# Kernel optimization log

Measured on AMD Instinct MI355X. Metric: run time of the kernel, lower is better.

## Reference

```python
import jax, jax.numpy as jnp
import numpy as np

N_NODES = 50000
N_EDGES = 800000
D = 128


def setup_inputs() -> dict:
    key = jax.random.key(0)
    ks = jax.random.split(key, 6)
    node_features = jax.random.normal(ks[0], (N_NODES, D), dtype=jnp.float32)
    edge_index = jax.random.randint(ks[1], (2, N_EDGES), 0, N_NODES, dtype=jnp.int64)
    s = 1.0 / np.sqrt(D)
    W1 = jax.random.normal(ks[2], (D, D), dtype=jnp.float32) * s
    b1 = jnp.zeros((D,), dtype=jnp.float32)
    W2 = jax.random.normal(ks[3], (D, D), dtype=jnp.float32) * s
    b2 = jnp.zeros((D,), dtype=jnp.float32)
    eta = jax.random.normal(ks[4], (1, 1), dtype=jnp.float32) * 0.5
    ln_gamma = jnp.ones((D,), dtype=jnp.float32)
    ln_beta = jnp.zeros((D,), dtype=jnp.float32)
    return {"node_features": node_features, "edge_index": edge_index,
            "W1": W1, "b1": b1, "W2": W2, "b2": b2, "eta": eta,
            "ln_gamma": ln_gamma, "ln_beta": ln_beta}


def _layer_norm(x, gamma, beta, eps=1e-5):
    mu = jnp.mean(x, axis=-1, keepdims=True)
    var = jnp.var(x, axis=-1, keepdims=True)
    return (x - mu) * jax.lax.rsqrt(var + eps) * gamma + beta


def reference(node_features, edge_index, W1, b1, W2, b2, eta, ln_gamma, ln_beta):
    initial = node_features
    src, dst = edge_index[0], edge_index[1]
    # gather neighbor features and sum-aggregate per destination node
    hu = node_features[src]                                   # [E, D]
    sum_hu = jax.ops.segment_sum(hu, dst, num_segments=node_features.shape[0])
    z = (1.0 + eta) * node_features + sum_hu                  # [N, D]
    # MLP: Linear -> ReLU -> Linear -> ReLU, then outer ReLU (idempotent)
    h = jax.nn.relu(z @ W1.T + b1)
    h = jax.nn.relu(h @ W2.T + b2)
    h = jax.nn.relu(h)
    h = _layer_norm(h, ln_gamma, ln_beta)                     # dropout p=0 -> identity
    return h + initial                                        # skip connection
```

## Files before the change

### kernel.cpp

```cpp
#include <hip/hip_runtime.h>

#define NN 50000
#define NE 800000
#define DD 128

typedef unsigned int u32;
typedef unsigned short u16;
typedef unsigned long long u64;
typedef __attribute__((ext_vector_type(8))) short bf16x8;
typedef __attribute__((ext_vector_type(4))) float f32x4;

__device__ __forceinline__ float bf2f(u16 u) {
    union { float f; u32 i; } v; v.i = ((u32)u) << 16; return v.f;
}
__device__ __forceinline__ u16 f2bf(float f) {
    u32 x = __float_as_uint(f);
    x += 0x7fffu + ((x >> 16) & 1u);
    return (u16)(x >> 16);
}

__global__ __launch_bounds__(64) void gin_detect(const u32* __restrict__ xw,
                                                 const u32* __restrict__ ew,
                                                 int* __restrict__ flags) {
    int lane = threadIdx.x;
    u32 w = xw[lane];
    u32 e8 = (w >> 7) & 0xFFu;
    bool bfOK = (e8 >= 100u && e8 <= 150u) || ((w & 0xFFFFu) == 0u);
    u64 m1 = __ballot(bfOK);
    bool oddZero = (ew[2 * lane + 1] == 0u);
    u64 m2 = __ballot(oddZero);
    if (lane == 0) {
        flags[0] = (__popcll(m1) >= 56) ? 1 : 0;
        flags[1] = (__popcll(m2) >= 60) ? 1 : 0;
    }
}

#define NB_TOBF ((NN * DD / 8) / 256)
#define NB_ZERO ((NN + 255) / 256)

__global__ __launch_bounds__(256) void gin_tobf_zero(const void* __restrict__ xv,
                                                     uint4* __restrict__ xb,
                                                     u32* __restrict__ deg,
                                                     const int* __restrict__ flags) {
    int b = blockIdx.x;
    int tid = threadIdx.x;
    if (b < NB_TOBF) {
        int i = b * 256 + tid;
        if (flags[0]) {
            xb[i] = ((const uint4*)xv)[i];
        } else {
            float4 a0 = ((const float4*)xv)[2 * i + 0];
            float4 a1 = ((const float4*)xv)[2 * i + 1];
            uint4 p;
            p.x = (u32)f2bf(a0.x) | ((u32)f2bf(a0.y) << 16);
            p.y = (u32)f2bf(a0.z) | ((u32)f2bf(a0.w) << 16);
            p.z = (u32)f2bf(a1.x) | ((u32)f2bf(a1.y) << 16);
            p.w = (u32)f2bf(a1.z) | ((u32)f2bf(a1.w) << 16);
            xb[i] = p;
        }
    } else {
        int i = (b - NB_TOBF) * 256 + tid;
        if (i < NN) deg[i] = 0u;
    }
}

__global__ __launch_bounds__(256) void gin_hist(const int* __restrict__ ei,
                                                u32* __restrict__ deg,
                                                u16* __restrict__ rank,
                                                u32* __restrict__ pck,
                                                const int* __restrict__ flags) {
    int e = blockIdx.x * 256 + threadIdx.x;
    if (e >= NE) return;
    int s, d;
    if (flags[1]) { s = ei[2 * e]; d = ei[2 * (NE + e)]; }
    else          { s = ei[e];     d = ei[NE + e]; }
    pck[e] = (u32)s | ((u32)d << 16);
    rank[e] = (u16)atomicAdd(&deg[d], 1u);
}

#define SCAN_CHUNK 2048
#define NSB ((NN + SCAN_CHUNK - 1) / SCAN_CHUNK)

__global__ __launch_bounds__(1024) void gin_scan1(const u32* __restrict__ deg,
                                                  u32* __restrict__ partials) {
    __shared__ u32 red[1024];
    int tid = threadIdx.x;
    int base = blockIdx.x * SCAN_CHUNK + tid * 2;
    u32 a = (base < NN) ? deg[base] : 0u;
    u32 b = (base + 1 < NN) ? deg[base + 1] : 0u;
    red[tid] = a + b;
    __syncthreads();
    for (int off = 512; off > 0; off >>= 1) {
        if (tid < off) red[tid] += red[tid + off];
        __syncthreads();
    }
    if (tid == 0) partials[blockIdx.x] = red[0];
}

__global__ __launch_bounds__(1024) void gin_scan3(const u32* __restrict__ deg,
                                                  const u32* __restrict__ partials,
                                                  u32* __restrict__ row_start) {
    __shared__ u32 sc[1024];
    __shared__ u32 chunk_base;
    int tid = threadIdx.x;
    if (tid < 64) {
        u32 v = (tid < NSB && tid < blockIdx.x) ? partials[tid] : 0u;
#pragma unroll
        for (int m = 32; m > 0; m >>= 1) v += __shfl_xor(v, m);
        if (tid == 0) chunk_base = v;
    }
    int base = blockIdx.x * SCAN_CHUNK + tid * 2;
    u32 a = (base < NN) ? deg[base] : 0u;
    u32 b = (base + 1 < NN) ? deg[base + 1] : 0u;
    u32 ts = a + b;
    sc[tid] = ts;
    __syncthreads();
    for (int off = 1; off < 1024; off <<= 1) {
        u32 v = (tid >= off) ? sc[tid - off] : 0u;
        __syncthreads();
        sc[tid] += v;
        __syncthreads();
    }
    u32 excl = sc[tid] - ts + chunk_base;
    if (base < NN) row_start[base] = excl;
    if (base + 1 < NN) row_start[base + 1] = excl + a;
}

__global__ __launch_bounds__(256) void gin_fill(const u32* __restrict__ pck,
                                                const u32* __restrict__ row_start,
                                                const u16* __restrict__ rank,
                                                u16* __restrict__ bs) {
    int e = blockIdx.x * 256 + threadIdx.x;
    if (e >= NE) return;
    u32 p = pck[e];
    u32 s = p & 0xffffu, d = p >> 16;
    bs[row_start[d] + (u32)rank[e]] = (u16)s;
}

__global__ __launch_bounds__(256) void gin_gather(const u32* __restrict__ xb,
                                                  const u16* __restrict__ bs,
                                                  const u32* __restrict__ row_start,
                                                  const u32* __restrict__ deg,
                                                  const void* __restrict__ etav,
                                                  u32* __restrict__ zb,
                                                  const int* __restrict__ flags) {
    int node = blockIdx.x * 4 + (threadIdx.x >> 6);
    if (node >= NN) return;
    const int lane = threadIdx.x & 63;
    const int h = lane >> 5;
    const int ll = lane & 31;
    float s = 1.0f + (flags[0] ? bf2f(((const u16*)etav)[0]) : ((const float*)etav)[0]);
    float w = h ? 0.f : s;

    uint2 sp = ((const uint2*)(xb + (size_t)node * 64))[ll];
    float a0 = bf2f((u16)(sp.x & 0xffffu)) * w;
    float a1 = bf2f((u16)(sp.x >> 16)) * w;
    float a2 = bf2f((u16)(sp.y & 0xffffu)) * w;
    float a3 = bf2f((u16)(sp.y >> 16)) * w;

#define ACC2(P) \
    a0 += bf2f((u16)((P).x & 0xffffu)); a1 += bf2f((u16)((P).x >> 16)); \
    a2 += bf2f((u16)((P).y & 0xffffu)); a3 += bf2f((u16)((P).y >> 16));

    u32 jb = row_start[node], je = jb + deg[node];
    u32 j = jb;
    for (; j + 15 < je; j += 16) {
        u32 i0 = bs[j + 0 + h],  i1 = bs[j + 2 + h],  i2 = bs[j + 4 + h],  i3 = bs[j + 6 + h];
        u32 i4 = bs[j + 8 + h],  i5 = bs[j + 10 + h], i6 = bs[j + 12 + h], i7 = bs[j + 14 + h];
        uint2 p0 = ((const uint2*)(xb + (size_t)i0 * 64))[ll];
        uint2 p1 = ((const uint2*)(xb + (size_t)i1 * 64))[ll];
        uint2 p2 = ((const uint2*)(xb + (size_t)i2 * 64))[ll];
        uint2 p3 = ((const uint2*)(xb + (size_t)i3 * 64))[ll];
        uint2 p4 = ((const uint2*)(xb + (size_t)i4 * 64))[ll];
        uint2 p5 = ((const uint2*)(xb + (size_t)i5 * 64))[ll];
        uint2 p6 = ((const uint2*)(xb + (size_t)i6 * 64))[ll];
        uint2 p7 = ((const uint2*)(xb + (size_t)i7 * 64))[ll];
        ACC2(p0) ACC2(p1) ACC2(p2) ACC2(p3) ACC2(p4) ACC2(p5) ACC2(p6) ACC2(p7)
    }
    for (; j + 3 < je; j += 4) {
        u32 i0 = bs[j + 0 + h], i1 = bs[j + 2 + h];
        uint2 p0 = ((const uint2*)(xb + (size_t)i0 * 64))[ll];
        uint2 p1 = ((const uint2*)(xb + (size_t)i1 * 64))[ll];
        ACC2(p0) ACC2(p1)
    }
    for (; j + 1 < je; j += 2) {
        u32 i0 = bs[j + h];
        uint2 p0 = ((const uint2*)(xb + (size_t)i0 * 64))[ll];
        ACC2(p0)
    }
    if (j < je && h == 0) {
        u32 i0 = bs[j];
        uint2 p0 = ((const uint2*)(xb + (size_t)i0 * 64))[ll];
        ACC2(p0)
    }
#undef ACC2
    a0 += __shfl_xor(a0, 32);
    a1 += __shfl_xor(a1, 32);
    a2 += __shfl_xor(a2, 32);
    a3 += __shfl_xor(a3, 32);
    if (h == 0) {
        uint2 o;
        o.x = (u32)f2bf(a0) | ((u32)f2bf(a1) << 16);
        o.y = (u32)f2bf(a2) | ((u32)f2bf(a3) << 16);
        ((uint2*)(zb + (size_t)node * 64))[ll] = o;
    }
}

__global__ __launch_bounds__(256) void gin_init(const void* __restrict__ xv,
                                                const void* __restrict__ etav,
                                                float* __restrict__ z,
                                                const int* __restrict__ flags) {
    int i = blockIdx.x * 256 + threadIdx.x;
    const int n8 = NN * DD / 8;
    if (i >= n8) return;
    const int fbf = flags[0];
    float s = 1.0f + (fbf ? bf2f(((const u16*)etav)[0]) : ((const float*)etav)[0]);
    float4 a, b;
    if (fbf) {
        uint4 p = ((const uint4*)xv)[i];
        a.x = bf2f((u16)(p.x & 0xffffu)); a.y = bf2f((u16)(p.x >> 16));
        a.z = bf2f((u16)(p.y & 0xffffu)); a.w = bf2f((u16)(p.y >> 16));
        b.x = bf2f((u16)(p.z & 0xffffu)); b.y = bf2f((u16)(p.z >> 16));
        b.z = bf2f((u16)(p.w & 0xffffu)); b.w = bf2f((u16)(p.w >> 16));
    } else {
        a = ((const float4*)xv)[2 * i + 0];
        b = ((const float4*)xv)[2 * i + 1];
    }
    a.x *= s; a.y *= s; a.z *= s; a.w *= s;
    b.x *= s; b.y *= s; b.z *= s; b.w *= s;
    ((float4*)z)[2 * i + 0] = a;
    ((float4*)z)[2 * i + 1] = b;
}

__global__ __launch_bounds__(256) void gin_scatter(const void* __restrict__ xv,
                                                   const int* __restrict__ ei,
                                                   float* __restrict__ z,
                                                   const int* __restrict__ flags) {
    int e = blockIdx.x * 4 + (threadIdx.x >> 6);
    if (e >= NE) return;
    const int fbf = flags[0];
    const int f64 = flags[1];
    int lane = threadIdx.x & 63;
    int s, d;
    if (f64) { s = ei[2 * e]; d = ei[2 * (NE + e)]; }
    else     { s = ei[e];     d = ei[NE + e]; }
    float v0, v1;
    if (fbf) {
        u32 p = ((const u32*)((const u16*)xv + (size_t)s * DD))[lane];
        v0 = bf2f((u16)(p & 0xffffu));
        v1 = bf2f((u16)(p >> 16));
    } else {
        float2 p = ((const float2*)((const float*)xv + (size_t)s * DD))[lane];
        v0 = p.x; v1 = p.y;
    }
    float* dst = z + (size_t)d * DD + 2 * lane;
    atomicAdd(dst + 0, v0);
    atomicAdd(dst + 1, v1);
}

#define TRM 64
#define NTM ((NN + TRM - 1) / TRM)

template <int FBF, int ZBF>
__global__ __launch_bounds__(512, 1) void gin_mlp(
    const void* __restrict__ zv, const void* __restrict__ xskip,
    const void* __restrict__ W1, const void* __restrict__ b1,
    const void* __restrict__ W2, const void* __restrict__ b2,
    const void* __restrict__ gamma, const void* __restrict__ beta,
    float* __restrict__ out, const int* __restrict__ flags) {
    if (flags[0] != FBF) return;

    __shared__ short s_w1[DD * DD];
    __shared__ short s_w2[DD * DD];
    __shared__ short s_zt[TRM * DD];
    __shared__ short s_h1[TRM * DD];
    __shared__ float s_h2[TRM * 132];

    const int tid = threadIdx.x;
    char* w1c = (char*)s_w1;
    char* w2c = (char*)s_w2;
    char* ztc = (char*)s_zt;
    char* h1c = (char*)s_h1;

    if (FBF) {
#pragma unroll
        for (int q = 0; q < 4; ++q) {
            int u = tid + q * 512;
            int row = u >> 4, cu = u & 15;
            uint4 a = ((const uint4*)W1)[u];
            uint4 c = ((const uint4*)W2)[u];
            int off = row * 256 + ((cu ^ (row & 7)) << 4);
            *(uint4*)(w1c + off) = a;
            *(uint4*)(w2c + off) = c;
        }
    } else {
#pragma unroll
        for (int q = 0; q < 4; ++q) {
            int u = tid + q * 512;
            int row = u >> 4, cu = u & 15;
            float4 a0 = ((const float4*)W1)[u * 2 + 0];
            float4 a1 = ((const float4*)W1)[u * 2 + 1];
            float4 c0 = ((const float4*)W2)[u * 2 + 0];
            float4 c1 = ((const float4*)W2)[u * 2 + 1];
            uint4 pa, pc;
            pa.x = (u32)f2bf(a0.x) | ((u32)f2bf(a0.y) << 16);
            pa.y = (u32)f2bf(a0.z) | ((u32)f2bf(a0.w) << 16);
            pa.z = (u32)f2bf(a1.x) | ((u32)f2bf(a1.y) << 16);
            pa.w = (u32)f2bf(a1.z) | ((u32)f2bf(a1.w) << 16);
            pc.x = (u32)f2bf(c0.x) | ((u32)f2bf(c0.y) << 16);
            pc.y = (u32)f2bf(c0.z) | ((u32)f2bf(c0.w) << 16);
            pc.z = (u32)f2bf(c1.x) | ((u32)f2bf(c1.y) << 16);
            pc.w = (u32)f2bf(c1.z) | ((u32)f2bf(c1.w) << 16);
            int off = row * 256 + ((cu ^ (row & 7)) << 4);
            *(uint4*)(w1c + off) = pa;
            *(uint4*)(w2c + off) = pc;
        }
    }

    const int lane = tid & 63;
    const int wid = tid >> 6;
    const int lrow = lane & 15;
    const int hi = lane >> 4;
    const int rstrip = wid & 3;
    const int nb = (wid >> 2) * 64;
    const int arow = rstrip * 16 + lrow;

    float b1v[4], b2v[4];
#pragma unroll
    for (int tt = 0; tt < 4; ++tt) {
        int j = nb + tt * 16 + lrow;
        b1v[tt] = FBF ? bf2f(((const u16*)b1)[j]) : ((const float*)b1)[j];
        b2v[tt] = FBF ? bf2f(((const u16*)b2)[j]) : ((const float*)b2)[j];
    }

    const int cg = tid & 31;
    const int rg = tid >> 5;
    const int r0 = rg * 4;
    float gv[4], bev[4];
    if (FBF) {
        uint2 pg = ((const uint2*)gamma)[cg];
        uint2 pe = ((const uint2*)beta)[cg];
        gv[0] = bf2f((u16)(pg.x & 0xffffu)); gv[1] = bf2f((u16)(pg.x >> 16));
        gv[2] = bf2f((u16)(pg.y & 0xffffu)); gv[3] = bf2f((u16)(pg.y >> 16));
        bev[0] = bf2f((u16)(pe.x & 0xffffu)); bev[1] = bf2f((u16)(pe.x >> 16));
        bev[2] = bf2f((u16)(pe.y & 0xffffu)); bev[3] = bf2f((u16)(pe.y >> 16));
    } else {
        float4 t3 = ((const float4*)gamma)[cg];
        float4 t4 = ((const float4*)beta)[cg];
        gv[0] = t3.x; gv[1] = t3.y; gv[2] = t3.z; gv[3] = t3.w;
        bev[0] = t4.x; bev[1] = t4.y; bev[2] = t4.z; bev[3] = t4.w;
    }

    for (int t = blockIdx.x; t < NTM; t += gridDim.x) {
        const int row0 = t * TRM;
        __syncthreads();
        if (ZBF) {
#pragma unroll
            for (int q = 0; q < 2; ++q) {
                int u = tid + q * 512;
                int row = u >> 4, cu = u & 15;
                int grow = row0 + row;
                uint4 p = {0u, 0u, 0u, 0u};
                if (grow < NN) p = ((const uint4*)zv)[(size_t)grow * 16 + cu];
                *(uint4*)(ztc + row * 256 + ((cu ^ (row & 7)) << 4)) = p;
            }
        } else {
#pragma unroll
            for (int q = 0; q < 2; ++q) {
                int u = tid + q * 512;
                int row = u >> 4, cu = u & 15;
                int grow = row0 + row;
                float4 a0 = {0.f, 0.f, 0.f, 0.f}, a1 = {0.f, 0.f, 0.f, 0.f};
                if (grow < NN) {
                    a0 = ((const float4*)zv)[(size_t)grow * 32 + cu * 2 + 0];
                    a1 = ((const float4*)zv)[(size_t)grow * 32 + cu * 2 + 1];
                }
                uint4 p;
                p.x = (u32)f2bf(a0.x) | ((u32)f2bf(a0.y) << 16);
                p.y = (u32)f2bf(a0.z) | ((u32)f2bf(a0.w) << 16);
                p.z = (u32)f2bf(a1.x) | ((u32)f2bf(a1.y) << 16);
                p.w = (u32)f2bf(a1.z) | ((u32)f2bf(a1.w) << 16);
                *(uint4*)(ztc + row * 256 + ((cu ^ (row & 7)) << 4)) = p;
            }
        }
        __syncthreads();

        f32x4 acc[4];
#pragma unroll
        for (int tt = 0; tt < 4; ++tt)
            acc[tt] = (f32x4){b1v[tt], b1v[tt], b1v[tt], b1v[tt]};
#pragma unroll
        for (int c = 0; c < 4; ++c) {
            bf16x8 af = *(const bf16x8*)(ztc + arow * 256 + (((c * 4 + hi) ^ (arow & 7)) << 4));
#pragma unroll
            for (int tt = 0; tt < 4; ++tt) {
                int brow = nb + tt * 16 + lrow;
                bf16x8 bfv = *(const bf16x8*)(w1c + brow * 256 + (((c * 4 + hi) ^ (brow & 7)) << 4));
                acc[tt] = __builtin_amdgcn_mfma_f32_16x16x32_bf16(af, bfv, acc[tt], 0, 0, 0);
            }
        }
#pragma unroll
        for (int tt = 0; tt < 4; ++tt) {
            int j = nb + tt * 16 + lrow;
            int jb2 = j * 2;
            int unit = jb2 >> 4, within = jb2 & 15;
#pragma unroll
            for (int qq = 0; qq < 4; ++qq) {
                int row = rstrip * 16 + hi * 4 + qq;
                u16 hb = f2bf(fmaxf(acc[tt][qq], 0.f));
                *(u16*)(h1c + row * 256 + ((unit ^ (row & 7)) << 4) + within) = hb;
            }
        }
        __syncthreads();
#pragma unroll
        for (int tt = 0; tt < 4; ++tt)
            acc[tt] = (f32x4){b2v[tt], b2v[tt], b2v[tt], b2v[tt]};
#pragma unroll
        for (int c = 0; c < 4; ++c) {
            bf16x8 af = *(const bf16x8*)(h1c + arow * 256 + (((c * 4 + hi) ^ (arow & 7)) << 4));
#pragma unroll
            for (int tt = 0; tt < 4; ++tt) {
                int brow = nb + tt * 16 + lrow;
                bf16x8 bfv = *(const bf16x8*)(w2c + brow * 256 + (((c * 4 + hi) ^ (brow & 7)) << 4));
                acc[tt] = __builtin_amdgcn_mfma_f32_16x16x32_bf16(af, bfv, acc[tt], 0, 0, 0);
            }
        }
#pragma unroll
        for (int tt = 0; tt < 4; ++tt) {
            int j = nb + tt * 16 + lrow;
#pragma unroll
            for (int qq = 0; qq < 4; ++qq) {
                int row = rstrip * 16 + hi * 4 + qq;
                s_h2[row * 132 + j] = fmaxf(acc[tt][qq], 0.f);
            }
        }
        __syncthreads();
#pragma unroll
        for (int r = 0; r < 4; ++r) {
            const float* hp = &s_h2[(r0 + r) * 132 + 4 * cg];
            float h0 = hp[0], h1 = hp[1], h2 = hp[2], h3 = hp[3];
            float s1 = h0 + h1 + h2 + h3;
            float s2 = h0 * h0 + h1 * h1 + h2 * h2 + h3 * h3;
#pragma unroll
            for (int m = 1; m <= 16; m <<= 1) {
                s1 += __shfl_xor(s1, m);
                s2 += __shfl_xor(s2, m);
            }
            float mean = s1 * (1.0f / DD);
            float var = s2 * (1.0f / DD) - mean * mean;
            float rs = rsqrtf(var + 1e-5f);
            int grow = row0 + r0 + r;
            if (grow < NN) {
                float xi[4];
                if (FBF || ZBF) {
                    uint2 px = ((const uint2*)((const u16*)xskip + (size_t)grow * DD))[cg];
                    xi[0] = bf2f((u16)(px.x & 0xffffu)); xi[1] = bf2f((u16)(px.x >> 16));
                    xi[2] = bf2f((u16)(px.y & 0xffffu)); xi[3] = bf2f((u16)(px.y >> 16));
                } else {
                    float4 px = ((const float4*)((const float*)xskip + (size_t)grow * DD))[cg];
                    xi[0] = px.x; xi[1] = px.y; xi[2] = px.z; xi[3] = px.w;
                }
                float4 o;
                o.x = (h0 - mean) * rs * gv[0] + bev[0] + xi[0];
                o.y = (h1 - mean) * rs * gv[1] + bev[1] + xi[1];
                o.z = (h2 - mean) * rs * gv[2] + bev[2] + xi[2];
                o.w = (h3 - mean) * rs * gv[3] + bev[3] + xi[3];
                ((float4*)(out + (size_t)grow * DD))[cg] = o;
            }
        }
    }
}

extern "C" void kernel_launch(void* const* d_in, const int* in_sizes, int n_in,
                              void* d_out, int out_size, void* d_ws, size_t ws_size,
                              hipStream_t stream) {
    const void* x = d_in[0];
    const int* ei = (const int*)d_in[1];
    const void* W1 = d_in[2];
    const void* b1 = d_in[3];
    const void* W2 = d_in[4];
    const void* b2 = d_in[5];
    const void* eta = d_in[6];
    const void* gamma = d_in[7];
    const void* beta = d_in[8];
    float* out = (float*)d_out;

    const size_t FLAGS_OFF = 0;
    const size_t PART_OFF = 64;
    const size_t Z_OFF = 256;
    const size_t ZB = (size_t)NN * DD * sizeof(float);
    const size_t XB_OFF = Z_OFF;
    const size_t ZBF_OFF = Z_OFF + (size_t)NN * DD * 2;
    const size_t DEG_OFF = Z_OFF + ZB;
    const size_t DEGB = 200192;
    const size_t RS_OFF = DEG_OFF + DEGB;
    const size_t RSB = 200448;
    const size_t BS_OFF = RS_OFF + RSB;
    const size_t BSB = (size_t)NE * sizeof(u16);
    const size_t RK_OFF = BS_OFF + BSB;
    const size_t RKB = (size_t)NE * sizeof(u16);
    const size_t PCK_OFF = RK_OFF + RKB;
    const size_t PCKB = (size_t)NE * sizeof(u32);
    const size_t TOT = PCK_OFF + PCKB;

    if (ws_size < Z_OFF + ZB) return;
    int* flags = (int*)((char*)d_ws + FLAGS_OFF);
    u32* partials = (u32*)((char*)d_ws + PART_OFF);

    gin_detect<<<1, 64, 0, stream>>>((const u32*)x, (const u32*)ei, flags);

    if (ws_size >= TOT) {
        u32* xb = (u32*)((char*)d_ws + XB_OFF);
        u32* zb = (u32*)((char*)d_ws + ZBF_OFF);
        u32* deg = (u32*)((char*)d_ws + DEG_OFF);
        u32* row_start = (u32*)((char*)d_ws + RS_OFF);
        u16* bs = (u16*)((char*)d_ws + BS_OFF);
        u16* rank = (u16*)((char*)d_ws + RK_OFF);
        u32* pck = (u32*)((char*)d_ws + PCK_OFF);
        gin_tobf_zero<<<NB_TOBF + NB_ZERO, 256, 0, stream>>>(x, (uint4*)xb, deg, flags);
        gin_hist<<<(NE + 255) / 256, 256, 0, stream>>>(ei, deg, rank, pck, flags);
        gin_scan1<<<NSB, 1024, 0, stream>>>(deg, partials);
        gin_scan3<<<NSB, 1024, 0, stream>>>(deg, partials, row_start);
        gin_fill<<<(NE + 255) / 256, 256, 0, stream>>>(pck, row_start, rank, bs);
        gin_gather<<<(NN + 3) / 4, 256, 0, stream>>>(xb, bs, row_start, deg, eta, zb, flags);
        gin_mlp<0, 1><<<256, 512, 0, stream>>>(zb, xb, W1, b1, W2, b2, gamma, beta, out, flags);
        gin_mlp<1, 1><<<256, 512, 0, stream>>>(zb, xb, W1, b1, W2, b2, gamma, beta, out, flags);
    } else {
        float* z = (float*)((char*)d_ws + Z_OFF);
        gin_init<<<(NN * DD / 8 + 255) / 256, 256, 0, stream>>>(x, eta, z, flags);
        gin_scatter<<<NE / 4, 256, 0, stream>>>(x, ei, z, flags);
        gin_mlp<0, 0><<<256, 512, 0, stream>>>(z, x, W1, b1, W2, b2, gamma, beta, out, flags);
        gin_mlp<1, 0><<<256, 512, 0, stream>>>(z, x, W1, b1, W2, b2, gamma, beta, out, flags);
    }
}
```

Measured before the change: 127.4 us.

## Fuse CSR neighbor gather into the MLP kernel via shared-memory tiles

The separate gather kernel is removed, and the persistent MLP kernel now gathers and aggregates neighbor rows for its 64-row tile directly into shared memory before the matmuls. This avoids writing and re-reading the bf16 aggregated z buffer in global memory and drops one kernel launch. In exchange, the irregular gather now runs with far fewer resident waves (256 blocks, one per CU), which reduces memory-latency hiding. Gather and MFMA phases are serialized within each tile.

```diff
diff --git a/kernel.cpp b/kernel.cpp
--- a/kernel.cpp
+++ b/kernel.cpp
@@ -137,133 +137,14 @@
     bs[row_start[d] + (u32)rank[e]] = (u16)s;
 }
 
-__global__ __launch_bounds__(256) void gin_gather(const u32* __restrict__ xb,
-                                                  const u16* __restrict__ bs,
-                                                  const u32* __restrict__ row_start,
-                                                  const u32* __restrict__ deg,
-                                                  const void* __restrict__ etav,
-                                                  u32* __restrict__ zb,
-                                                  const int* __restrict__ flags) {
-    int node = blockIdx.x * 4 + (threadIdx.x >> 6);
-    if (node >= NN) return;
-    const int lane = threadIdx.x & 63;
-    const int h = lane >> 5;
-    const int ll = lane & 31;
-    float s = 1.0f + (flags[0] ? bf2f(((const u16*)etav)[0]) : ((const float*)etav)[0]);
-    float w = h ? 0.f : s;
-
-    uint2 sp = ((const uint2*)(xb + (size_t)node * 64))[ll];
-    float a0 = bf2f((u16)(sp.x & 0xffffu)) * w;
-    float a1 = bf2f((u16)(sp.x >> 16)) * w;
-    float a2 = bf2f((u16)(sp.y & 0xffffu)) * w;
-    float a3 = bf2f((u16)(sp.y >> 16)) * w;
-
-#define ACC2(P) \
-    a0 += bf2f((u16)((P).x & 0xffffu)); a1 += bf2f((u16)((P).x >> 16)); \
-    a2 += bf2f((u16)((P).y & 0xffffu)); a3 += bf2f((u16)((P).y >> 16));
-
-    u32 jb = row_start[node], je = jb + deg[node];
-    u32 j = jb;
-    for (; j + 15 < je; j += 16) {
-        u32 i0 = bs[j + 0 + h],  i1 = bs[j + 2 + h],  i2 = bs[j + 4 + h],  i3 = bs[j + 6 + h];
-        u32 i4 = bs[j + 8 + h],  i5 = bs[j + 10 + h], i6 = bs[j + 12 + h], i7 = bs[j + 14 + h];
-        uint2 p0 = ((const uint2*)(xb + (size_t)i0 * 64))[ll];
-        uint2 p1 = ((const uint2*)(xb + (size_t)i1 * 64))[ll];
-        uint2 p2 = ((const uint2*)(xb + (size_t)i2 * 64))[ll];
-        uint2 p3 = ((const uint2*)(xb + (size_t)i3 * 64))[ll];
-        uint2 p4 = ((const uint2*)(xb + (size_t)i4 * 64))[ll];
-        uint2 p5 = ((const uint2*)(xb + (size_t)i5 * 64))[ll];
-        uint2 p6 = ((const uint2*)(xb + (size_t)i6 * 64))[ll];
-        uint2 p7 = ((const uint2*)(xb + (size_t)i7 * 64))[ll];
-        ACC2(p0) ACC2(p1) ACC2(p2) ACC2(p3) ACC2(p4) ACC2(p5) ACC2(p6) ACC2(p7)
-    }
-    for (; j + 3 < je; j += 4) {
-        u32 i0 = bs[j + 0 + h], i1 = bs[j + 2 + h];
-        uint2 p0 = ((const uint2*)(xb + (size_t)i0 * 64))[ll];
-        uint2 p1 = ((const uint2*)(xb + (size_t)i1 * 64))[ll];
-        ACC2(p0) ACC2(p1)
-    }
-    for (; j + 1 < je; j += 2) {
-        u32 i0 = bs[j + h];
-        uint2 p0 = ((const uint2*)(xb + (size_t)i0 * 64))[ll];
-        ACC2(p0)
-    }
-    if (j < je && h == 0) {
-        u32 i0 = bs[j];
-        uint2 p0 = ((const uint2*)(xb + (size_t)i0 * 64))[ll];
-        ACC2(p0)
-    }
-#undef ACC2
-    a0 += __shfl_xor(a0, 32);
-    a1 += __shfl_xor(a1, 32);
-    a2 += __shfl_xor(a2, 32);
-    a3 += __shfl_xor(a3, 32);
-    if (h == 0) {
-        uint2 o;
-        o.x = (u32)f2bf(a0) | ((u32)f2bf(a1) << 16);
-        o.y = (u32)f2bf(a2) | ((u32)f2bf(a3) << 16);
-        ((uint2*)(zb + (size_t)node * 64))[ll] = o;
-    }
-}
-
-__global__ __launch_bounds__(256) void gin_init(const void* __restrict__ xv,
-                                                const void* __restrict__ etav,
-                                                float* __restrict__ z,
-                                                const int* __restrict__ flags) {
-    int i = blockIdx.x * 256 + threadIdx.x;
-    const int n8 = NN * DD / 8;
-    if (i >= n8) return;
-    const int fbf = flags[0];
-    float s = 1.0f + (fbf ? bf2f(((const u16*)etav)[0]) : ((const float*)etav)[0]);
-    float4 a, b;
-    if (fbf) {
-        uint4 p = ((const uint4*)xv)[i];
-        a.x = bf2f((u16)(p.x & 0xffffu)); a.y = bf2f((u16)(p.x >> 16));
-        a.z = bf2f((u16)(p.y & 0xffffu)); a.w = bf2f((u16)(p.y >> 16));
-        b.x = bf2f((u16)(p.z & 0xffffu)); b.y = bf2f((u16)(p.z >> 16));
-        b.z = bf2f((u16)(p.w & 0xffffu)); b.w = bf2f((u16)(p.w >> 16));
-    } else {
-        a = ((const float4*)xv)[2 * i + 0];
-        b = ((const float4*)xv)[2 * i + 1];
-    }
-    a.x *= s; a.y *= s; a.z *= s; a.w *= s;
-    b.x *= s; b.y *= s; b.z *= s; b.w *= s;
-    ((float4*)z)[2 * i + 0] = a;
-    ((float4*)z)[2 * i + 1] = b;
-}
-
-__global__ __launch_bounds__(256) void gin_scatter(const void* __restrict__ xv,
-                                                   const int* __restrict__ ei,
-                                                   float* __restrict__ z,
-                                                   const int* __restrict__ flags) {
-    int e = blockIdx.x * 4 + (threadIdx.x >> 6);
-    if (e >= NE) return;
-    const int fbf = flags[0];
-    const int f64 = flags[1];
-    int lane = threadIdx.x & 63;
-    int s, d;
-    if (f64) { s = ei[2 * e]; d = ei[2 * (NE + e)]; }
-    else     { s = ei[e];     d = ei[NE + e]; }
-    float v0, v1;
-    if (fbf) {
-        u32 p = ((const u32*)((const u16*)xv + (size_t)s * DD))[lane];
-        v0 = bf2f((u16)(p & 0xffffu));
-        v1 = bf2f((u16)(p >> 16));
-    } else {
-        float2 p = ((const float2*)((const float*)xv + (size_t)s * DD))[lane];
-        v0 = p.x; v1 = p.y;
-    }
-    float* dst = z + (size_t)d * DD + 2 * lane;
-    atomicAdd(dst + 0, v0);
-    atomicAdd(dst + 1, v1);
-}
-
 #define TRM 64
 #define NTM ((NN + TRM - 1) / TRM)
 
-template <int FBF, int ZBF>
-__global__ __launch_bounds__(512, 1) void gin_mlp(
-    const void* __restrict__ zv, const void* __restrict__ xskip,
+template <int FBF>
+__global__ __launch_bounds__(512, 1) void gin_gmlp(
+    const u32* __restrict__ xb, const u16* __restrict__ bs,
+    const u32* __restrict__ row_start, const u32* __restrict__ deg,
+    const void* __restrict__ etav,
     const void* __restrict__ W1, const void* __restrict__ b1,
     const void* __restrict__ W2, const void* __restrict__ b2,
     const void* __restrict__ gamma, const void* __restrict__ beta,
@@ -319,6 +200,10 @@
 
     const int lane = tid & 63;
     const int wid = tid >> 6;
+    const int gh = lane >> 5;
+    const int gll = lane & 31;
+    float es = 1.0f + (FBF ? bf2f(((const u16*)etav)[0]) : ((const float*)etav)[0]);
+    const float w0 = gh ? 0.f : es;
     const int lrow = lane & 15;
     const int hi = lane >> 4;
     const int rstrip = wid & 3;
@@ -354,34 +239,307 @@
     for (int t = blockIdx.x; t < NTM; t += gridDim.x) {
         const int row0 = t * TRM;
         __syncthreads();
-        if (ZBF) {
-#pragma unroll
-            for (int q = 0; q < 2; ++q) {
-                int u = tid + q * 512;
-                int row = u >> 4, cu = u & 15;
-                int grow = row0 + row;
-                uint4 p = {0u, 0u, 0u, 0u};
-                if (grow < NN) p = ((const uint4*)zv)[(size_t)grow * 16 + cu];
-                *(uint4*)(ztc + row * 256 + ((cu ^ (row & 7)) << 4)) = p;
-            }
-        } else {
-#pragma unroll
-            for (int q = 0; q < 2; ++q) {
-                int u = tid + q * 512;
-                int row = u >> 4, cu = u & 15;
-                int grow = row0 + row;
-                float4 a0 = {0.f, 0.f, 0.f, 0.f}, a1 = {0.f, 0.f, 0.f, 0.f};
-                if (grow < NN) {
-                    a0 = ((const float4*)zv)[(size_t)grow * 32 + cu * 2 + 0];
-                    a1 = ((const float4*)zv)[(size_t)grow * 32 + cu * 2 + 1];
+        for (int nd = 0; nd < 8; ++nd) {
+            const int row = wid * 8 + nd;
+            const int node = row0 + row;
+            float a0 = 0.f, a1 = 0.f, a2 = 0.f, a3 = 0.f;
+            if (node < NN) {
+                uint2 sp = ((const uint2*)(xb + (size_t)node * 64))[gll];
+                a0 = bf2f((u16)(sp.x & 0xffffu)) * w0;
+                a1 = bf2f((u16)(sp.x >> 16)) * w0;
+                a2 = bf2f((u16)(sp.y & 0xffffu)) * w0;
+                a3 = bf2f((u16)(sp.y >> 16)) * w0;
+#define ACC2(P) \
+    a0 += bf2f((u16)((P).x & 0xffffu)); a1 += bf2f((u16)((P).x >> 16)); \
+    a2 += bf2f((u16)((P).y & 0xffffu)); a3 += bf2f((u16)((P).y >> 16));
+                u32 jb = row_start[node], je = jb + deg[node];
+                u32 j = jb;
+                for (; j + 15 < je; j += 16) {
+                    u32 i0 = bs[j + 0 + gh],  i1 = bs[j + 2 + gh],  i2 = bs[j + 4 + gh],  i3 = bs[j + 6 + gh];
+                    u32 i4 = bs[j + 8 + gh],  i5 = bs[j + 10 + gh], i6 = bs[j + 12 + gh], i7 = bs[j + 14 + gh];
+                    uint2 p0 = ((const uint2*)(xb + (size_t)i0 * 64))[gll];
+                    uint2 p1 = ((const uint2*)(xb + (size_t)i1 * 64))[gll];
+                    uint2 p2 = ((const uint2*)(xb + (size_t)i2 * 64))[gll];
+                    uint2 p3 = ((const uint2*)(xb + (size_t)i3 * 64))[gll];
+                    uint2 p4 = ((const uint2*)(xb + (size_t)i4 * 64))[gll];
+                    uint2 p5 = ((const uint2*)(xb + (size_t)i5 * 64))[gll];
+                    uint2 p6 = ((const uint2*)(xb + (size_t)i6 * 64))[gll];
+                    uint2 p7 = ((const uint2*)(xb + (size_t)i7 * 64))[gll];
+                    ACC2(p0) ACC2(p1) ACC2(p2) ACC2(p3) ACC2(p4) ACC2(p5) ACC2(p6) ACC2(p7)
                 }
-                uint4 p;
-                p.x = (u32)f2bf(a0.x) | ((u32)f2bf(a0.y) << 16);
-                p.y = (u32)f2bf(a0.z) | ((u32)f2bf(a0.w) << 16);
-                p.z = (u32)f2bf(a1.x) | ((u32)f2bf(a1.y) << 16);
-                p.w = (u32)f2bf(a1.z) | ((u32)f2bf(a1.w) << 16);
-                *(uint4*)(ztc + row * 256 + ((cu ^ (row & 7)) << 4)) = p;
-            }
+                for (; j + 3 < je; j += 4) {
+                    u32 i0 = bs[j + 0 + gh], i1 = bs[j + 2 + gh];
+                    uint2 p0 = ((const uint2*)(xb + (size_t)i0 * 64))[gll];
+                    uint2 p1 = ((const uint2*)(xb + (size_t)i1 * 64))[gll];
+                    ACC2(p0) ACC2(p1)
+                }
+                for (; j + 1 < je; j += 2) {
+                    u32 i0 = bs[j + gh];
+                    uint2 p0 = ((const uint2*)(xb + (size_t)i0 * 64))[gll];
+                    ACC2(p0)
+                }
+                if (j < je && gh == 0) {
+                    u32 i0 = bs[j];
+                    uint2 p0 = ((const uint2*)(xb + (size_t)i0 * 64))[gll];
+                    ACC2(p0)
+                }
+#undef ACC2
+            }
+            a0 += __shfl_xor(a0, 32);
+            a1 += __shfl_xor(a1, 32);
+            a2 += __shfl_xor(a2, 32);
+            a3 += __shfl_xor(a3, 32);
+            if (gh == 0) {
+                uint2 o;
+                o.x = (u32)f2bf(a0) | ((u32)f2bf(a1) << 16);
+                o.y = (u32)f2bf(a2) | ((u32)f2bf(a3) << 16);
+                int unit = gll >> 1;
+                *(uint2*)(ztc + row * 256 + ((unit ^ (row & 7)) << 4) + (gll & 1) * 8) = o;
+            }
+        }
+        __syncthreads();
+
+        f32x4 acc[4];
+#pragma unroll
+        for (int tt = 0; tt < 4; ++tt)
+            acc[tt] = (f32x4){b1v[tt], b1v[tt], b1v[tt], b1v[tt]};
+#pragma unroll
+        for (int c = 0; c < 4; ++c) {
+            bf16x8 af = *(const bf16x8*)(ztc + arow * 256 + (((c * 4 + hi) ^ (arow & 7)) << 4));
+#pragma unroll
+            for (int tt = 0; tt < 4; ++tt) {
+                int brow = nb + tt * 16 + lrow;
+                bf16x8 bfv = *(const bf16x8*)(w1c + brow * 256 + (((c * 4 + hi) ^ (brow & 7)) << 4));
+                acc[tt] = __builtin_amdgcn_mfma_f32_16x16x32_bf16(af, bfv, acc[tt], 0, 0, 0);
+            }
+        }
+#pragma unroll
+        for (int tt = 0; tt < 4; ++tt) {
+            int j = nb + tt * 16 + lrow;
+            int jb2 = j * 2;
+            int unit = jb2 >> 4, within = jb2 & 15;
+#pragma unroll
+            for (int qq = 0; qq < 4; ++qq) {
+                int row = rstrip * 16 + hi * 4 + qq;
+                u16 hb = f2bf(fmaxf(acc[tt][qq], 0.f));
+                *(u16*)(h1c + row * 256 + ((unit ^ (row & 7)) << 4) + within) = hb;
+            }
+        }
+        __syncthreads();
+#pragma unroll
+        for (int tt = 0; tt < 4; ++tt)
+            acc[tt] = (f32x4){b2v[tt], b2v[tt], b2v[tt], b2v[tt]};
+#pragma unroll
+        for (int c = 0; c < 4; ++c) {
+            bf16x8 af = *(const bf16x8*)(h1c + arow * 256 + (((c * 4 + hi) ^ (arow & 7)) << 4));
+#pragma unroll
+            for (int tt = 0; tt < 4; ++tt) {
+                int brow = nb + tt * 16 + lrow;
+                bf16x8 bfv = *(const bf16x8*)(w2c + brow * 256 + (((c * 4 + hi) ^ (brow & 7)) << 4));
+                acc[tt] = __builtin_amdgcn_mfma_f32_16x16x32_bf16(af, bfv, acc[tt], 0, 0, 0);
+            }
+        }
+#pragma unroll
+        for (int tt = 0; tt < 4; ++tt) {
+            int j = nb + tt * 16 + lrow;
+#pragma unroll
+            for (int qq = 0; qq < 4; ++qq) {
+                int row = rstrip * 16 + hi * 4 + qq;
+                s_h2[row * 132 + j] = fmaxf(acc[tt][qq], 0.f);
+            }
+        }
+        __syncthreads();
+#pragma unroll
+        for (int r = 0; r < 4; ++r) {
+            const float* hp = &s_h2[(r0 + r) * 132 + 4 * cg];
+            float h0 = hp[0], h1 = hp[1], h2 = hp[2], h3 = hp[3];
+            float s1 = h0 + h1 + h2 + h3;
+            float s2 = h0 * h0 + h1 * h1 + h2 * h2 + h3 * h3;
+#pragma unroll
+            for (int m = 1; m <= 16; m <<= 1) {
+                s1 += __shfl_xor(s1, m);
+                s2 += __shfl_xor(s2, m);
+            }
+            float mean = s1 * (1.0f / DD);
+            float var = s2 * (1.0f / DD) - mean * mean;
+            float rs = rsqrtf(var + 1e-5f);
+            int grow = row0 + r0 + r;
+            if (grow < NN) {
+                uint2 px = ((const uint2*)((const u16*)xb + (size_t)grow * DD))[cg];
+                float xi0 = bf2f((u16)(px.x & 0xffffu)), xi1 = bf2f((u16)(px.x >> 16));
+                float xi2 = bf2f((u16)(px.y & 0xffffu)), xi3 = bf2f((u16)(px.y >> 16));
+                float4 o;
+                o.x = (h0 - mean) * rs * gv[0] + bev[0] + xi0;
+                o.y = (h1 - mean) * rs * gv[1] + bev[1] + xi1;
+                o.z = (h2 - mean) * rs * gv[2] + bev[2] + xi2;
+                o.w = (h3 - mean) * rs * gv[3] + bev[3] + xi3;
+                ((float4*)(out + (size_t)grow * DD))[cg] = o;
+            }
+        }
+    }
+}
+
+__global__ __launch_bounds__(256) void gin_init(const void* __restrict__ xv,
+                                                const void* __restrict__ etav,
+                                                float* __restrict__ z,
+                                                const int* __restrict__ flags) {
+    int i = blockIdx.x * 256 + threadIdx.x;
+    const int n8 = NN * DD / 8;
+    if (i >= n8) return;
+    const int fbf = flags[0];
+    float s = 1.0f + (fbf ? bf2f(((const u16*)etav)[0]) : ((const float*)etav)[0]);
+    float4 a, b;
+    if (fbf) {
+        uint4 p = ((const uint4*)xv)[i];
+        a.x = bf2f((u16)(p.x & 0xffffu)); a.y = bf2f((u16)(p.x >> 16));
+        a.z = bf2f((u16)(p.y & 0xffffu)); a.w = bf2f((u16)(p.y >> 16));
+        b.x = bf2f((u16)(p.z & 0xffffu)); b.y = bf2f((u16)(p.z >> 16));
+        b.z = bf2f((u16)(p.w & 0xffffu)); b.w = bf2f((u16)(p.w >> 16));
+    } else {
+        a = ((const float4*)xv)[2 * i + 0];
+        b = ((const float4*)xv)[2 * i + 1];
+    }
+    a.x *= s; a.y *= s; a.z *= s; a.w *= s;
+    b.x *= s; b.y *= s; b.z *= s; b.w *= s;
+    ((float4*)z)[2 * i + 0] = a;
+    ((float4*)z)[2 * i + 1] = b;
+}
+
+__global__ __launch_bounds__(256) void gin_scatter(const void* __restrict__ xv,
+                                                   const int* __restrict__ ei,
+                                                   float* __restrict__ z,
+                                                   const int* __restrict__ flags) {
+    int e = blockIdx.x * 4 + (threadIdx.x >> 6);
+    if (e >= NE) return;
+    const int fbf = flags[0];
+    const int f64 = flags[1];
+    int lane = threadIdx.x & 63;
+    int s, d;
+    if (f64) { s = ei[2 * e]; d = ei[2 * (NE + e)]; }
+    else     { s = ei[e];     d = ei[NE + e]; }
+    float v0, v1;
+    if (fbf) {
+        u32 p = ((const u32*)((const u16*)xv + (size_t)s * DD))[lane];
+        v0 = bf2f((u16)(p & 0xffffu));
+        v1 = bf2f((u16)(p >> 16));
+    } else {
+        float2 p = ((const float2*)((const float*)xv + (size_t)s * DD))[lane];
+        v0 = p.x; v1 = p.y;
+    }
+    float* dst = z + (size_t)d * DD + 2 * lane;
+    atomicAdd(dst + 0, v0);
+    atomicAdd(dst + 1, v1);
+}
+
+template <int FBF>
+__global__ __launch_bounds__(512, 1) void gin_mlp(
+    const float* __restrict__ zv, const void* __restrict__ xskip,
+    const void* __restrict__ W1, const void* __restrict__ b1,
+    const void* __restrict__ W2, const void* __restrict__ b2,
+    const void* __restrict__ gamma, const void* __restrict__ beta,
+    float* __restrict__ out, const int* __restrict__ flags) {
+    if (flags[0] != FBF) return;
+
+    __shared__ short s_w1[DD * DD];
+    __shared__ short s_w2[DD * DD];
+    __shared__ short s_zt[TRM * DD];
+    __shared__ short s_h1[TRM * DD];
+    __shared__ float s_h2[TRM * 132];
+
+    const int tid = threadIdx.x;
+    char* w1c = (char*)s_w1;
+    char* w2c = (char*)s_w2;
+    char* ztc = (char*)s_zt;
+    char* h1c = (char*)s_h1;
+
+    if (FBF) {
+#pragma unroll
+        for (int q = 0; q < 4; ++q) {
+            int u = tid + q * 512;
+            int row = u >> 4, cu = u & 15;
+            uint4 a = ((const uint4*)W1)[u];
+            uint4 c = ((const uint4*)W2)[u];
+            int off = row * 256 + ((cu ^ (row & 7)) << 4);
+            *(uint4*)(w1c + off) = a;
+            *(uint4*)(w2c + off) = c;
+        }
+    } else {
+#pragma unroll
+        for (int q = 0; q < 4; ++q) {
+            int u = tid + q * 512;
+            int row = u >> 4, cu = u & 15;
+            float4 a0 = ((const float4*)W1)[u * 2 + 0];
+            float4 a1 = ((const float4*)W1)[u * 2 + 1];
+            float4 c0 = ((const float4*)W2)[u * 2 + 0];
+            float4 c1 = ((const float4*)W2)[u * 2 + 1];
+            uint4 pa, pc;
+            pa.x = (u32)f2bf(a0.x) | ((u32)f2bf(a0.y) << 16);
+            pa.y = (u32)f2bf(a0.z) | ((u32)f2bf(a0.w) << 16);
+            pa.z = (u32)f2bf(a1.x) | ((u32)f2bf(a1.y) << 16);
+            pa.w = (u32)f2bf(a1.z) | ((u32)f2bf(a1.w) << 16);
+            pc.x = (u32)f2bf(c0.x) | ((u32)f2bf(c0.y) << 16);
+            pc.y = (u32)f2bf(c0.z) | ((u32)f2bf(c0.w) << 16);
+            pc.z = (u32)f2bf(c1.x) | ((u32)f2bf(c1.y) << 16);
+            pc.w = (u32)f2bf(c1.z) | ((u32)f2bf(c1.w) << 16);
+            int off = row * 256 + ((cu ^ (row & 7)) << 4);
+            *(uint4*)(w1c + off) = pa;
+            *(uint4*)(w2c + off) = pc;
+        }
+    }
+
+    const int lane = tid & 63;
+    const int wid = tid >> 6;
+    const int lrow = lane & 15;
+    const int hi = lane >> 4;
+    const int rstrip = wid & 3;
+    const int nb = (wid >> 2) * 64;
+    const int arow = rstrip * 16 + lrow;
+
+    float b1v[4], b2v[4];
+#pragma unroll
+    for (int tt = 0; tt < 4; ++tt) {
+        int j = nb + tt * 16 + lrow;
+        b1v[tt] = FBF ? bf2f(((const u16*)b1)[j]) : ((const float*)b1)[j];
+        b2v[tt] = FBF ? bf2f(((const u16*)b2)[j]) : ((const float*)b2)[j];
+    }
+
+    const int cg = tid & 31;
+    const int rg = tid >> 5;
+    const int r0 = rg * 4;
+    float gv[4], bev[4];
+    if (FBF) {
+        uint2 pg = ((const uint2*)gamma)[cg];
+        uint2 pe = ((const uint2*)beta)[cg];
+        gv[0] = bf2f((u16)(pg.x & 0xffffu)); gv[1] = bf2f((u16)(pg.x >> 16));
+        gv[2] = bf2f((u16)(pg.y & 0xffffu)); gv[3] = bf2f((u16)(pg.y >> 16));
+        bev[0] = bf2f((u16)(pe.x & 0xffffu)); bev[1] = bf2f((u16)(pe.x >> 16));
+        bev[2] = bf2f((u16)(pe.y & 0xffffu)); bev[3] = bf2f((u16)(pe.y >> 16));
+    } else {
+        float4 t3 = ((const float4*)gamma)[cg];
+        float4 t4 = ((const float4*)beta)[cg];
+        gv[0] = t3.x; gv[1] = t3.y; gv[2] = t3.z; gv[3] = t3.w;
+        bev[0] = t4.x; bev[1] = t4.y; bev[2] = t4.z; bev[3] = t4.w;
+    }
+
+    for (int t = blockIdx.x; t < NTM; t += gridDim.x) {
+        const int row0 = t * TRM;
+        __syncthreads();
+#pragma unroll
+        for (int q = 0; q < 2; ++q) {
+            int u = tid + q * 512;
+            int row = u >> 4, cu = u & 15;
+            int grow = row0 + row;
+            float4 a0 = {0.f, 0.f, 0.f, 0.f}, a1 = {0.f, 0.f, 0.f, 0.f};
+            if (grow < NN) {
+                a0 = ((const float4*)zv)[(size_t)grow * 32 + cu * 2 + 0];
+                a1 = ((const float4*)zv)[(size_t)grow * 32 + cu * 2 + 1];
+            }
+            uint4 p;
+            p.x = (u32)f2bf(a0.x) | ((u32)f2bf(a0.y) << 16);
+            p.y = (u32)f2bf(a0.z) | ((u32)f2bf(a0.w) << 16);
+            p.z = (u32)f2bf(a1.x) | ((u32)f2bf(a1.y) << 16);
+            p.w = (u32)f2bf(a1.z) | ((u32)f2bf(a1.w) << 16);
+            *(uint4*)(ztc + row * 256 + ((cu ^ (row & 7)) << 4)) = p;
         }
         __syncthreads();
 
@@ -452,7 +610,7 @@
             int grow = row0 + r0 + r;
             if (grow < NN) {
                 float xi[4];
-                if (FBF || ZBF) {
+                if (FBF) {
                     uint2 px = ((const uint2*)((const u16*)xskip + (size_t)grow * DD))[cg];
                     xi[0] = bf2f((u16)(px.x & 0xffffu)); xi[1] = bf2f((u16)(px.x >> 16));
                     xi[2] = bf2f((u16)(px.y & 0xffffu)); xi[3] = bf2f((u16)(px.y >> 16));
@@ -490,7 +648,6 @@
     const size_t Z_OFF = 256;
     const size_t ZB = (size_t)NN * DD * sizeof(float);
     const size_t XB_OFF = Z_OFF;
-    const size_t ZBF_OFF = Z_OFF + (size_t)NN * DD * 2;
     const size_t DEG_OFF = Z_OFF + ZB;
     const size_t DEGB = 200192;
     const size_t RS_OFF = DEG_OFF + DEGB;
@@ -511,7 +668,6 @@
 
     if (ws_size >= TOT) {
         u32* xb = (u32*)((char*)d_ws + XB_OFF);
-        u32* zb = (u32*)((char*)d_ws + ZBF_OFF);
         u32* deg = (u32*)((char*)d_ws + DEG_OFF);
         u32* row_start = (u32*)((char*)d_ws + RS_OFF);
         u16* bs = (u16*)((char*)d_ws + BS_OFF);
@@ -522,14 +678,13 @@
         gin_scan1<<<NSB, 1024, 0, stream>>>(deg, partials);
         gin_scan3<<<NSB, 1024, 0, stream>>>(deg, partials, row_start);
         gin_fill<<<(NE + 255) / 256, 256, 0, stream>>>(pck, row_start, rank, bs);
-        gin_gather<<<(NN + 3) / 4, 256, 0, stream>>>(xb, bs, row_start, deg, eta, zb, flags);
-        gin_mlp<0, 1><<<256, 512, 0, stream>>>(zb, xb, W1, b1, W2, b2, gamma, beta, out, flags);
-        gin_mlp<1, 1><<<256, 512, 0, stream>>>(zb, xb, W1, b1, W2, b2, gamma, beta, out, flags);
+        gin_gmlp<0><<<256, 512, 0, stream>>>(xb, bs, row_start, deg, eta, W1, b1, W2, b2, gamma, beta, out, flags);
+        gin_gmlp<1><<<256, 512, 0, stream>>>(xb, bs, row_start, deg, eta, W1, b1, W2, b2, gamma, beta, out, flags);
     } else {
         float* z = (float*)((char*)d_ws + Z_OFF);
         gin_init<<<(NN * DD / 8 + 255) / 256, 256, 0, stream>>>(x, eta, z, flags);
         gin_scatter<<<NE / 4, 256, 0, stream>>>(x, ei, z, flags);
-        gin_mlp<0, 0><<<256, 512, 0, stream>>>(z, x, W1, b1, W2, b2, gamma, beta, out, flags);
-        gin_mlp<1, 0><<<256, 512, 0, stream>>>(z, x, W1, b1, W2, b2, gamma, beta, out, flags);
-    }
-}
+        gin_mlp<0><<<256, 512, 0, stream>>>(z, x, W1, b1, W2, b2, gamma, beta, out, flags);
+        gin_mlp<1><<<256, 512, 0, stream>>>(z, x, W1, b1, W2, b2, gamma, beta, out, flags);
+    }
+}
```

Result: slower. 184.7 us (+45.0%).
